# Optimization experiments

Hardware: AMD Instinct MI355X
Metric: run time of the kernel (lower is better)

The kernel has to match this reference:

```python
import jax, jax.numpy as jnp
import numpy as np

NUM_QUBITS = 4
SHOTS = 1000
BATCH = 8192
IN_SIZE = 4096
OUT_SIZE = 4096


def setup_inputs() -> dict:
    key = jax.random.key(0)
    k_x, k_w, k_b, k_q = jax.random.split(key, 4)
    x = jax.random.normal(k_x, (BATCH, IN_SIZE), dtype=jnp.float32)
    W = jax.random.normal(k_w, (OUT_SIZE, IN_SIZE), dtype=jnp.float32) * (1.0 / np.sqrt(IN_SIZE))
    b = jax.random.normal(k_b, (OUT_SIZE,), dtype=jnp.float32) * 0.01
    # Each shot's measurement outcome: num_qubits independent uniform bits
    # == one uniform integer in [0, 2**num_qubits).
    quantum_outcomes = jax.random.randint(k_q, (BATCH, SHOTS), 0, 2 ** NUM_QUBITS, dtype=jnp.int32)
    return {"x": x, "W": W, "b": b, "quantum_outcomes": quantum_outcomes}


def reference(x, W, b, quantum_outcomes):
    # classical path: nn.Linear
    classical = jnp.einsum("bi,oi->bo", x, W) + b  # [B, OUT]
    # normalized by max outcome, broadcast across the output dim.
    max_outcome = float(2 ** NUM_QUBITS - 1)
    expectation = jnp.mean(quantum_outcomes.astype(jnp.float32), axis=1) / max_outcome  # [B]
    return classical + expectation[:, None]
```

## Files before the change

### kernel.cpp

```cpp
#include <hip/hip_runtime.h>
#include <hip/hip_bf16.h>

typedef __attribute__((ext_vector_type(8))) short short8;
typedef __attribute__((ext_vector_type(4))) float f32x4;
typedef unsigned short ushort_t;

#define BM 128
#define BN 128
#define BK 64

__device__ __forceinline__ ushort_t f2bf_rne(float f) {
    unsigned u = __float_as_uint(f);
    u += 0x7FFF + ((u >> 16) & 1);
    return (ushort_t)(u >> 16);
}

__device__ __forceinline__ short8 pack8(float4 a, float4 b) {
    short8 r;
    r[0] = (short)f2bf_rne(a.x); r[1] = (short)f2bf_rne(a.y);
    r[2] = (short)f2bf_rne(a.z); r[3] = (short)f2bf_rne(a.w);
    r[4] = (short)f2bf_rne(b.x); r[5] = (short)f2bf_rne(b.y);
    r[6] = (short)f2bf_rne(b.z); r[7] = (short)f2bf_rne(b.w);
    return r;
}

__global__ void prep_kernel(const float* __restrict__ x, ushort_t* __restrict__ xb,
                            const float* __restrict__ w, ushort_t* __restrict__ wb,
                            const int* __restrict__ q, float* __restrict__ e,
                            int blocks_x, int blocks_w, int shots) {
    int bid = blockIdx.x;
    if (bid < blocks_x + blocks_w) {
        const float* src; ushort_t* dst; long long base;
        if (bid < blocks_x) { src = x; dst = xb; base = (long long)bid * blockDim.x; }
        else { src = w; dst = wb; base = (long long)(bid - blocks_x) * blockDim.x; }
        long long i = base + threadIdx.x;
        float4 a0 = ((const float4*)src)[4 * i];
        float4 a1 = ((const float4*)src)[4 * i + 1];
        float4 a2 = ((const float4*)src)[4 * i + 2];
        float4 a3 = ((const float4*)src)[4 * i + 3];
        ((short8*)dst)[2 * i]     = pack8(a0, a1);
        ((short8*)dst)[2 * i + 1] = pack8(a2, a3);
    } else {
        int eb = bid - (blocks_x + blocks_w);
        int row = eb * 4 + (threadIdx.x >> 6);
        int lane = threadIdx.x & 63;
        const int* rp = q + (long long)row * shots;
        int s = 0;
        for (int j = lane; j < shots; j += 64) s += rp[j];
        #pragma unroll
        for (int off = 32; off; off >>= 1) s += __shfl_down(s, off, 64);
        if (lane == 0) e[row] = (float)s * (1.0f / (1000.0f * 15.0f));
    }
}

__global__ __launch_bounds__(256, 2)
void gemm_kernel(const ushort_t* __restrict__ A, const ushort_t* __restrict__ B,
                 const float* __restrict__ bias, const float* __restrict__ expect,
                 float* __restrict__ C, int M, int N, int K) {
    __shared__ ushort_t As[BM * BK];
    __shared__ ushort_t Bs[BN * BK];

    int pid = blockIdx.x;
    const int xcd = pid & 7;
    const int p   = pid >> 3;
    int pid_n = xcd * 4 + (p & 3);
    int pid_m = p >> 2;

    const int tid  = threadIdx.x;
    const int lane = tid & 63;
    const int wave = tid >> 6;
    const int wm = (wave >> 1) * 64;
    const int wn = (wave & 1) * 64;

    const int srow = tid >> 3;
    const int slot = tid & 7;
    const int gchunk = slot ^ (srow & 7);

    const ushort_t* a_ptr = A + (long long)pid_m * BM * K + gchunk * 8;
    const ushort_t* b_ptr = B + (long long)pid_n * BN * K + gchunk * 8;

    f32x4 acc[4][4];
    #pragma unroll
    for (int i = 0; i < 4; i++)
        #pragma unroll
        for (int j = 0; j < 4; j++)
            acc[i][j] = (f32x4)(0.0f);

    const int quad = lane >> 4;
    const int l15  = lane & 15;
    const int rlow = l15 & 7;

    for (int k0 = 0; k0 < K; k0 += BK) {
        #pragma unroll
        for (int s = 0; s < 4; s++) {
            int row = srow + s * 32;
            __builtin_amdgcn_global_load_lds(
                (const __attribute__((address_space(1))) unsigned int*)(a_ptr + (long long)row * K + k0),
                (__attribute__((address_space(3))) unsigned int*)(As + row * BK + slot * 8),
                16, 0, 0);
        }
        #pragma unroll
        for (int s = 0; s < 4; s++) {
            int row = srow + s * 32;
            __builtin_amdgcn_global_load_lds(
                (const __attribute__((address_space(1))) unsigned int*)(b_ptr + (long long)row * K + k0),
                (__attribute__((address_space(3))) unsigned int*)(Bs + row * BK + slot * 8),
                16, 0, 0);
        }
        __syncthreads();

        #pragma unroll
        for (int ks = 0; ks < 2; ks++) {
            int q = ks * 4 + quad;
            int sw = (q ^ rlow) * 8;
            short8 af[4], bf[4];
            #pragma unroll
            for (int i = 0; i < 4; i++) {
                af[i] = *(const short8*)(As + (wm + i * 16 + l15) * BK + sw);
                bf[i] = *(const short8*)(Bs + (wn + i * 16 + l15) * BK + sw);
            }
            #pragma unroll
            for (int i = 0; i < 4; i++)
                #pragma unroll
                for (int j = 0; j < 4; j++)
                    acc[i][j] = __builtin_amdgcn_mfma_f32_16x16x32_bf16(
                        af[i], bf[j], acc[i][j], 0, 0, 0);
        }
        __syncthreads();
    }

    long long row0 = (long long)pid_m * BM + wm;
    int col0 = pid_n * BN + wn;
    #pragma unroll
    for (int j = 0; j < 4; j++) {
        int col = col0 + j * 16 + l15;
        float bj = bias[col];
        #pragma unroll
        for (int i = 0; i < 4; i++) {
            #pragma unroll
            for (int r = 0; r < 4; r++) {
                long long row = row0 + i * 16 + quad * 4 + r;
                C[row * N + col] = acc[i][j][r] + bj + expect[row];
            }
        }
    }
}

__global__ void expect_kernel(const int* __restrict__ q, float* __restrict__ e,
                              int rows, int shots) {
    int row = blockIdx.x * (blockDim.x >> 6) + (threadIdx.x >> 6);
    int lane = threadIdx.x & 63;
    if (row >= rows) return;
    const int* rp = q + (long long)row * shots;
    int s = 0;
    for (int j = lane; j < shots; j += 64) s += rp[j];
    #pragma unroll
    for (int off = 32; off; off >>= 1) s += __shfl_down(s, off, 64);
    if (lane == 0) e[row] = (float)s * (1.0f / (1000.0f * 15.0f));
}

__global__ __launch_bounds__(256, 2)
void gemm_f32stage_kernel(const float* __restrict__ A, const float* __restrict__ B,
                          const float* __restrict__ bias, const float* __restrict__ expect,
                          float* __restrict__ C, int M, int N, int K) {
    __shared__ ushort_t As[BM * BK];
    __shared__ ushort_t Bs[BN * BK];

    int pid = blockIdx.x;
    const int xcd = pid & 7;
    const int p   = pid >> 3;
    int pid_n = xcd * 4 + (p & 3);
    int pid_m = p >> 2;

    const int tid  = threadIdx.x;
    const int lane = tid & 63;
    const int wave = tid >> 6;
    const int wm = (wave >> 1) * 64;
    const int wn = (wave & 1) * 64;

    const int srow = tid >> 1;
    const int chalf = (tid & 1) * 4;

    const float* a_base = A + ((long long)pid_m * BM + srow) * K + chalf * 8;
    const float* b_base = B + ((long long)pid_n * BN + srow) * K + chalf * 8;

    f32x4 acc[4][4];
    #pragma unroll
    for (int i = 0; i < 4; i++)
        #pragma unroll
        for (int j = 0; j < 4; j++)
            acc[i][j] = (f32x4)(0.0f);

    const int quad = lane >> 4;
    const int l15  = lane & 15;
    const int rlow = l15 & 7;

    for (int k0 = 0; k0 < K; k0 += BK) {
        {
            const float4* ap = (const float4*)(a_base + k0);
            const float4* bp = (const float4*)(b_base + k0);
            float4 fa[8], fb[8];
            #pragma unroll
            for (int c = 0; c < 8; c++) { fa[c] = ap[c]; fb[c] = bp[c]; }
            #pragma unroll
            for (int c = 0; c < 4; c++) {
                int sl = ((chalf + c) ^ (srow & 7)) * 8;
                *(short8*)(As + srow * BK + sl) = pack8(fa[2*c], fa[2*c+1]);
                *(short8*)(Bs + srow * BK + sl) = pack8(fb[2*c], fb[2*c+1]);
            }
        }
        __syncthreads();

        #pragma unroll
        for (int ks = 0; ks < 2; ks++) {
            int q = ks * 4 + quad;
            int sw = (q ^ rlow) * 8;
            short8 af[4], bf[4];
            #pragma unroll
            for (int i = 0; i < 4; i++) {
                af[i] = *(const short8*)(As + (wm + i * 16 + l15) * BK + sw);
                bf[i] = *(const short8*)(Bs + (wn + i * 16 + l15) * BK + sw);
            }
            #pragma unroll
            for (int i = 0; i < 4; i++)
                #pragma unroll
                for (int j = 0; j < 4; j++)
                    acc[i][j] = __builtin_amdgcn_mfma_f32_16x16x32_bf16(
                        af[i], bf[j], acc[i][j], 0, 0, 0);
        }
        __syncthreads();
    }

    long long row0 = (long long)pid_m * BM + wm;
    int col0 = pid_n * BN + wn;
    #pragma unroll
    for (int j = 0; j < 4; j++) {
        int col = col0 + j * 16 + l15;
        float bj = bias[col];
        #pragma unroll
        for (int i = 0; i < 4; i++) {
            #pragma unroll
            for (int r = 0; r < 4; r++) {
                long long row = row0 + i * 16 + quad * 4 + r;
                C[row * N + col] = acc[i][j][r] + bj + expect[row];
            }
        }
    }
}

extern "C" void kernel_launch(void* const* d_in, const int* in_sizes, int n_in,
                              void* d_out, int out_size, void* d_ws, size_t ws_size,
                              hipStream_t stream) {
    const float* x = (const float*)d_in[0];
    const float* W = (const float*)d_in[1];
    const float* b = (const float*)d_in[2];
    const int*   q = (const int*)d_in[3];
    float* out = (float*)d_out;

    const int M = 8192, N = 4096, K = 4096, SHOTS = 1000;

    float* expect = (float*)d_ws;
    size_t need = 32768 + (size_t)M * K * 2 + (size_t)N * K * 2;

    if (ws_size >= need) {
        ushort_t* xb = (ushort_t*)((char*)d_ws + 32768);
        ushort_t* wb = xb + (size_t)M * K;
        int blocks_x = (int)((long long)M * K / 16 / 256);
        int blocks_w = (int)((long long)N * K / 16 / 256);
        int blocks_e = M / 4;
        prep_kernel<<<blocks_x + blocks_w + blocks_e, 256, 0, stream>>>(
            x, xb, W, wb, q, expect, blocks_x, blocks_w, SHOTS);
        gemm_kernel<<<(M / BM) * (N / BN), 256, 0, stream>>>(xb, wb, b, expect, out, M, N, K);
    } else {
        expect_kernel<<<M / 4, 256, 0, stream>>>(q, expect, M, SHOTS);
        gemm_f32stage_kernel<<<(M / BM) * (N / BN), 256, 0, stream>>>(x, W, b, expect, out, M, N, K);
    }
}
```

Baseline: 543.2 us.

## Drop bf16 prepass and convert fp32 operands inside the GEMM

Removes the separate prep kernel that converted x and W to bf16 in workspace, and always uses the GEMM variant that loads fp32 tiles and converts them to bf16 in registers before staging to LDS. It also vectorises the per-row shot reduction with int4 loads. The goal is to avoid the extra write and re-read of the bf16 copies. In exchange the GEMM reads twice the bytes per tile, reconverts each tile once per reuse, and loses the direct global-to-LDS async load path.

```diff
diff --git a/kernel.cpp b/kernel.cpp
--- a/kernel.cpp
+++ b/kernel.cpp
@@ -24,145 +24,27 @@
     return r;
 }
 
-__global__ void prep_kernel(const float* __restrict__ x, ushort_t* __restrict__ xb,
-                            const float* __restrict__ w, ushort_t* __restrict__ wb,
-                            const int* __restrict__ q, float* __restrict__ e,
-                            int blocks_x, int blocks_w, int shots) {
-    int bid = blockIdx.x;
-    if (bid < blocks_x + blocks_w) {
-        const float* src; ushort_t* dst; long long base;
-        if (bid < blocks_x) { src = x; dst = xb; base = (long long)bid * blockDim.x; }
-        else { src = w; dst = wb; base = (long long)(bid - blocks_x) * blockDim.x; }
-        long long i = base + threadIdx.x;
-        float4 a0 = ((const float4*)src)[4 * i];
-        float4 a1 = ((const float4*)src)[4 * i + 1];
-        float4 a2 = ((const float4*)src)[4 * i + 2];
-        float4 a3 = ((const float4*)src)[4 * i + 3];
-        ((short8*)dst)[2 * i]     = pack8(a0, a1);
-        ((short8*)dst)[2 * i + 1] = pack8(a2, a3);
-    } else {
-        int eb = bid - (blocks_x + blocks_w);
-        int row = eb * 4 + (threadIdx.x >> 6);
-        int lane = threadIdx.x & 63;
-        const int* rp = q + (long long)row * shots;
-        int s = 0;
-        for (int j = lane; j < shots; j += 64) s += rp[j];
-        #pragma unroll
-        for (int off = 32; off; off >>= 1) s += __shfl_down(s, off, 64);
-        if (lane == 0) e[row] = (float)s * (1.0f / (1000.0f * 15.0f));
-    }
-}
-
-__global__ __launch_bounds__(256, 2)
-void gemm_kernel(const ushort_t* __restrict__ A, const ushort_t* __restrict__ B,
-                 const float* __restrict__ bias, const float* __restrict__ expect,
-                 float* __restrict__ C, int M, int N, int K) {
-    __shared__ ushort_t As[BM * BK];
-    __shared__ ushort_t Bs[BN * BK];
-
-    int pid = blockIdx.x;
-    const int xcd = pid & 7;
-    const int p   = pid >> 3;
-    int pid_n = xcd * 4 + (p & 3);
-    int pid_m = p >> 2;
-
-    const int tid  = threadIdx.x;
-    const int lane = tid & 63;
-    const int wave = tid >> 6;
-    const int wm = (wave >> 1) * 64;
-    const int wn = (wave & 1) * 64;
-
-    const int srow = tid >> 3;
-    const int slot = tid & 7;
-    const int gchunk = slot ^ (srow & 7);
-
-    const ushort_t* a_ptr = A + (long long)pid_m * BM * K + gchunk * 8;
-    const ushort_t* b_ptr = B + (long long)pid_n * BN * K + gchunk * 8;
-
-    f32x4 acc[4][4];
-    #pragma unroll
-    for (int i = 0; i < 4; i++)
-        #pragma unroll
-        for (int j = 0; j < 4; j++)
-            acc[i][j] = (f32x4)(0.0f);
-
-    const int quad = lane >> 4;
-    const int l15  = lane & 15;
-    const int rlow = l15 & 7;
-
-    for (int k0 = 0; k0 < K; k0 += BK) {
-        #pragma unroll
-        for (int s = 0; s < 4; s++) {
-            int row = srow + s * 32;
-            __builtin_amdgcn_global_load_lds(
-                (const __attribute__((address_space(1))) unsigned int*)(a_ptr + (long long)row * K + k0),
-                (__attribute__((address_space(3))) unsigned int*)(As + row * BK + slot * 8),
-                16, 0, 0);
-        }
-        #pragma unroll
-        for (int s = 0; s < 4; s++) {
-            int row = srow + s * 32;
-            __builtin_amdgcn_global_load_lds(
-                (const __attribute__((address_space(1))) unsigned int*)(b_ptr + (long long)row * K + k0),
-                (__attribute__((address_space(3))) unsigned int*)(Bs + row * BK + slot * 8),
-                16, 0, 0);
-        }
-        __syncthreads();
-
-        #pragma unroll
-        for (int ks = 0; ks < 2; ks++) {
-            int q = ks * 4 + quad;
-            int sw = (q ^ rlow) * 8;
-            short8 af[4], bf[4];
-            #pragma unroll
-            for (int i = 0; i < 4; i++) {
-                af[i] = *(const short8*)(As + (wm + i * 16 + l15) * BK + sw);
-                bf[i] = *(const short8*)(Bs + (wn + i * 16 + l15) * BK + sw);
-            }
-            #pragma unroll
-            for (int i = 0; i < 4; i++)
-                #pragma unroll
-                for (int j = 0; j < 4; j++)
-                    acc[i][j] = __builtin_amdgcn_mfma_f32_16x16x32_bf16(
-                        af[i], bf[j], acc[i][j], 0, 0, 0);
-        }
-        __syncthreads();
-    }
-
-    long long row0 = (long long)pid_m * BM + wm;
-    int col0 = pid_n * BN + wn;
-    #pragma unroll
-    for (int j = 0; j < 4; j++) {
-        int col = col0 + j * 16 + l15;
-        float bj = bias[col];
-        #pragma unroll
-        for (int i = 0; i < 4; i++) {
-            #pragma unroll
-            for (int r = 0; r < 4; r++) {
-                long long row = row0 + i * 16 + quad * 4 + r;
-                C[row * N + col] = acc[i][j][r] + bj + expect[row];
-            }
-        }
-    }
-}
-
 __global__ void expect_kernel(const int* __restrict__ q, float* __restrict__ e,
                               int rows, int shots) {
     int row = blockIdx.x * (blockDim.x >> 6) + (threadIdx.x >> 6);
     int lane = threadIdx.x & 63;
     if (row >= rows) return;
-    const int* rp = q + (long long)row * shots;
+    const int4* rp4 = (const int4*)(q + (long long)row * shots);
+    int nvec = shots >> 2;
     int s = 0;
-    for (int j = lane; j < shots; j += 64) s += rp[j];
+    for (int j = lane; j < nvec; j += 64) {
+        int4 v = rp4[j];
+        s += v.x + v.y + v.z + v.w;
+    }
     #pragma unroll
     for (int off = 32; off; off >>= 1) s += __shfl_down(s, off, 64);
     if (lane == 0) e[row] = (float)s * (1.0f / (1000.0f * 15.0f));
 }
 
 __global__ __launch_bounds__(256, 2)
-void gemm_f32stage_kernel(const float* __restrict__ A, const float* __restrict__ B,
-                          const float* __restrict__ bias, const float* __restrict__ expect,
-                          float* __restrict__ C, int M, int N, int K) {
+void gemm_fused_kernel(const float* __restrict__ A, const float* __restrict__ B,
+                       const float* __restrict__ bias, const float* __restrict__ expect,
+                       float* __restrict__ C, int M, int N, int K) {
     __shared__ ushort_t As[BM * BK];
     __shared__ ushort_t Bs[BN * BK];
 
@@ -260,19 +142,7 @@
     const int M = 8192, N = 4096, K = 4096, SHOTS = 1000;
 
     float* expect = (float*)d_ws;
-    size_t need = 32768 + (size_t)M * K * 2 + (size_t)N * K * 2;
 
-    if (ws_size >= need) {
-        ushort_t* xb = (ushort_t*)((char*)d_ws + 32768);
-        ushort_t* wb = xb + (size_t)M * K;
-        int blocks_x = (int)((long long)M * K / 16 / 256);
-        int blocks_w = (int)((long long)N * K / 16 / 256);
-        int blocks_e = M / 4;
-        prep_kernel<<<blocks_x + blocks_w + blocks_e, 256, 0, stream>>>(
-            x, xb, W, wb, q, expect, blocks_x, blocks_w, SHOTS);
-        gemm_kernel<<<(M / BM) * (N / BN), 256, 0, stream>>>(xb, wb, b, expect, out, M, N, K);
-    } else {
-        expect_kernel<<<M / 4, 256, 0, stream>>>(q, expect, M, SHOTS);
-        gemm_f32stage_kernel<<<(M / BM) * (N / BN), 256, 0, stream>>>(x, W, b, expect, out, M, N, K);
-    }
+    expect_kernel<<<M / 4, 256, 0, stream>>>(q, expect, M, SHOTS);
+    gemm_fused_kernel<<<(M / BM) * (N / BN), 256, 0, stream>>>(x, W, b, expect, out, M, N, K);
 }
```

Result: slower. 1.197 ms (+120.3%).
